# Kernel optimization log

Measured on AMD Instinct MI355X. Metric: run time of the kernel, lower is better.

## Reference

```python
import jax, jax.numpy as jnp
import numpy as np

H, DK, DV = 4, 64, 64        # heads, key/value head dims (hidden=256)
M, TOPK = 4, 2               # num memories, router top-k
GN, EPS, COND_SCALE = 16.0, 1e-5, 1.0


def setup_inputs() -> dict:
    key = jax.random.key(0)
    ks = jax.random.split(key, 12)
    B, Q, K, D = 8, 64, 256, 256
    w = lambda k, shape, fan: jax.random.normal(k, shape, jnp.float32) / np.sqrt(fan).astype(np.float32)
    return {
        "query": jax.random.normal(ks[0], (B, Q, D), jnp.float32),
        "keyval": jax.random.normal(ks[1], (B, K, D), jnp.float32),
        "attention_mask_kv": jnp.ones((B, K), jnp.int32),
        "W_cond": w(ks[2], (D, D), D),
        "W_q": w(ks[3], (D, H * DK), D),
        "W_k": w(ks[4], (D, H * DK), D),
        "W_v": w(ks[5], (D, H * DV), D),
        "W_gk1": w(ks[6], (D, 16), D),
        "W_gk2": w(ks[7], (16, H * DK), 16),
        "b_gk2": jnp.zeros((H * DK,), jnp.float32),
        "W_router": w(ks[8], (D, M), D),
        "norm_w": jnp.ones((DV,), jnp.float32),
        "W_o": w(ks[9], (H * DV, D), H * DV),
    }


def _mem_last(q_last, k, v, gk, sel, wgt):
    """Last-token output of one gated linear-attention memory.
    S_t = diag(exp(gk_t)) S_{t-1} + k_t v_t^T ; o_T = q_T S_T.
    q_last: (N,H,DK); k,gk: (N,K,H,DK); v: (N,K,H,DV); sel,wgt: (N,K)."""
    k_e = k * sel[:, :, None, None]
    v_e = v * wgt[:, :, None, None]
    gk_e = gk * sel[:, :, None, None]          # unselected tokens: no decay, no update
    G = jnp.cumsum(gk_e, axis=1)               # (N,K,H,DK), log decays
    decay = jnp.exp(G[:, -1:, :, :] - G)       # remaining decay to last step, <= 1
    s = jnp.einsum('nhd,nthd->nth', q_last, k_e * decay)
    return jnp.einsum('nth,nthv->nhv', s, v_e)


def reference(query, keyval, attention_mask_kv, W_cond, W_q, W_k, W_v,
              W_gk1, W_gk2, b_gk2, W_router, norm_w, W_o):
    B, Q, D = query.shape
    K = keyval.shape[1]
    N = B * Q
    # broadcast KV expansion + cond injection
    cond = (query @ W_cond) * COND_SCALE                         # (B,Q,D)
    x = (keyval[:, None, :, :] + cond[:, :, None, :]).reshape(N, K, D)
    m = jnp.broadcast_to(attention_mask_kv[:, None, :].astype(x.dtype), (B, Q, K)).reshape(N, K)
    # projections
    q = (x @ W_q).reshape(N, K, H, DK)
    k = (x @ W_k).reshape(N, K, H, DK) * m[:, :, None, None]
    v = (x @ W_v).reshape(N, K, H, DV) * m[:, :, None, None]
    gk = (jax.nn.log_sigmoid(x @ W_gk1 @ W_gk2 + b_gk2) / GN).reshape(N, K, H, DK)
    gk = gk * m[:, :, None, None]
    # router: softmax -> top-k -> renormalize
    router_logits = (x @ W_router).reshape(N * K, M)
    probs = jax.nn.softmax(router_logits, axis=-1)
    topv, topi = jax.lax.top_k(probs, TOPK)
    topv = topv / jnp.sum(topv, axis=-1, keepdims=True)
    w_mem = jnp.sum(jax.nn.one_hot(topi, M, dtype=x.dtype) * topv[..., None], axis=-2)
    w_mem = w_mem.reshape(N, K, M)
    # shared memory (always on) + routed memories
    q_last = q[:, -1]
    ones = jnp.ones((N, K), x.dtype)
    o = _mem_last(q_last, k, v, gk, ones, ones)
    for e in range(M):
        we = w_mem[:, :, e]
        o = o + _mem_last(q_last, k, v, gk, (we > 0).astype(x.dtype), we)
    # per-head RMSNorm + output projection
    o = o * jax.lax.rsqrt(jnp.mean(o * o, axis=-1, keepdims=True) + EPS) * norm_w
    out = (o.reshape(N, H * DV) @ W_o).reshape(B, Q, D)
    return out, router_logits
```

## Files before the change

### kernel.cpp

```cpp
#include <hip/hip_runtime.h>
#include <math.h>

#define Bb   8
#define Qq   64
#define Kk   256
#define Dd   256
#define Nn   (Bb * Qq)
#define GNi  0.0625f
#define EPSf 1e-5f

__device__ __forceinline__ float wred(float x) {
#pragma unroll
    for (int off = 32; off > 0; off >>= 1)
        x += __shfl_xor(x, off, 64);
    return x;
}

template<int R>
__device__ __forceinline__ void gemm64(
    const float* __restrict__ A, int lda,
    const float* __restrict__ B0, const float* __restrict__ B1,
    const float* __restrict__ B2, const float* __restrict__ B3,
    int bn, int Kc, float (&acc)[R][16], float* As, float* Ws)
{
    const int tid = threadIdx.x;
    const int aRow = tid >> 2, aCol = (tid & 3) * 4;
    const int wr = tid >> 4, wcb = (tid & 15) * 4;
    const int ty = tid >> 4, tx = tid & 15;
    const float* Bp[4] = {B0, B1, B2, B3};

    float4 rA = *(const float4*)(A + (size_t)aRow * lda + aCol);
    float4 rW[R];
#pragma unroll
    for (int r = 0; r < R; ++r)
        rW[r] = *(const float4*)(Bp[r] + (size_t)wr * 256 + bn + wcb);

    for (int k0 = 0; k0 < Kc; k0 += 16) {
        __syncthreads();
        As[(aCol + 0) * 68 + aRow] = rA.x;
        As[(aCol + 1) * 68 + aRow] = rA.y;
        As[(aCol + 2) * 68 + aRow] = rA.z;
        As[(aCol + 3) * 68 + aRow] = rA.w;
#pragma unroll
        for (int r = 0; r < R; ++r)
            *(float4*)&Ws[r * 1088 + wr * 68 + wcb] = rW[r];
        __syncthreads();
        if (k0 + 16 < Kc) {
            rA = *(const float4*)(A + (size_t)aRow * lda + k0 + 16 + aCol);
#pragma unroll
            for (int r = 0; r < R; ++r)
                rW[r] = *(const float4*)(Bp[r] + (size_t)(k0 + 16 + wr) * 256 + bn + wcb);
        }
#pragma unroll
        for (int kk = 0; kk < 16; ++kk) {
            const float4 a4 = *(const float4*)&As[kk * 68 + ty * 4];
            const float av[4] = {a4.x, a4.y, a4.z, a4.w};
#pragma unroll
            for (int r = 0; r < R; ++r) {
                const float4 b4 = *(const float4*)&Ws[r * 1088 + kk * 68 + tx * 4];
                const float bw[4] = {b4.x, b4.y, b4.z, b4.w};
#pragma unroll
                for (int i = 0; i < 4; ++i)
#pragma unroll
                    for (int j = 0; j < 4; ++j)
                        acc[r][i * 4 + j] = fmaf(av[i], bw[j], acc[r][i * 4 + j]);
            }
        }
    }
}

__global__ __launch_bounds__(256) void prep(
    const float* __restrict__ query, const float* __restrict__ keyval,
    const float* __restrict__ W_cond, const float* __restrict__ Wg1,
    const float* __restrict__ Wg2, const float* __restrict__ Wr,
    const float* __restrict__ Wq,
    float* __restrict__ cond, float* __restrict__ Wg,
    float* __restrict__ KVr, float* __restrict__ KVq8)
{
    __shared__ float lds[2 * 1088];
    const int id = blockIdx.x;
    const int tid = threadIdx.x;

    if (id < 48) {
        float acc[1][16] = {};
        const int ty = tid >> 4, tx = tid & 15;
        if (id < 32) {
            const int bm = (id >> 2) * 64, bn = (id & 3) * 64;
            gemm64<1>(query + (size_t)bm * Dd, Dd, W_cond, nullptr, nullptr, nullptr,
                      bn, Dd, acc, lds, lds + 1088);
#pragma unroll
            for (int i = 0; i < 4; ++i)
                *(float4*)&cond[(size_t)(bm + ty * 4 + i) * Dd + bn + tx * 4] =
                    make_float4(acc[0][i * 4 + 0], acc[0][i * 4 + 1],
                                acc[0][i * 4 + 2], acc[0][i * 4 + 3]);
        } else {
            const int id3 = id - 32;
            const int bm = (id3 >> 2) * 64, bn = (id3 & 3) * 64;
            gemm64<1>(Wg1 + (size_t)bm * 16, 16, Wg2, nullptr, nullptr, nullptr,
                      bn, 16, acc, lds, lds + 1088);
#pragma unroll
            for (int i = 0; i < 4; ++i)
                *(float4*)&Wg[(size_t)(bm + ty * 4 + i) * Dd + bn + tx * 4] =
                    make_float4(acc[0][i * 4 + 0], acc[0][i * 4 + 1],
                                acc[0][i * 4 + 2], acc[0][i * 4 + 3]);
        }
        return;
    }
    if (id < 80) {
        const int idx = (id - 48) * 256 + tid;
        const int row = idx >> 2, col = idx & 3;
        float a = 0.f;
        for (int k = 0; k < 256; ++k)
            a = fmaf(keyval[(size_t)row * Dd + k], Wr[(size_t)k * 4 + col], a);
        KVr[idx] = a;
        return;
    }
    for (int b8 = 0; b8 < 8; ++b8)
        lds[b8 * 256 + tid] = keyval[((size_t)b8 * Kk + 255) * Dd + tid];
    __syncthreads();
    float a8[8] = {};
    for (int k = 0; k < 256; ++k) {
        const float wq = Wq[(size_t)k * Dd + tid];
#pragma unroll
        for (int b8 = 0; b8 < 8; ++b8)
            a8[b8] = fmaf(lds[b8 * 256 + k], wq, a8[b8]);
    }
    for (int b8 = 0; b8 < 8; ++b8)
        KVq8[b8 * 256 + tid] = a8[b8];
}

__global__ __launch_bounds__(256) void maingemm(
    const float* __restrict__ keyval, const float* __restrict__ cond,
    const float* __restrict__ Wq, const float* __restrict__ Wk,
    const float* __restrict__ Wv, const float* __restrict__ Wg,
    const float* __restrict__ Wr,
    float* __restrict__ KVi, float* __restrict__ Cbi, float* __restrict__ Cr)
{
    __shared__ float lds[5 * 1088];
    const int id = blockIdx.x;
    const int tid = threadIdx.x;
    const int ty = tid >> 4, tx = tid & 15;

    if (id < 128) {
        const int bm = (id >> 2) * 64;
        const int bn = (id & 3) * 64;
        float acc[3][16] = {};
        gemm64<3>(keyval + (size_t)bm * Dd, Dd, Wk, Wv, Wg, nullptr,
                  bn, Dd, acc, lds, lds + 1088);
#pragma unroll
        for (int i = 0; i < 4; ++i) {
            const size_t rowo = (size_t)(bm + ty * 4 + i) * 1024;
#pragma unroll
            for (int j = 0; j < 4; ++j)
                *(float4*)&KVi[rowo + (size_t)(bn + tx * 4 + j) * 4] =
                    make_float4(acc[0][i * 4 + j], acc[1][i * 4 + j],
                                acc[2][i * 4 + j], 0.f);
        }
    } else if (id < 160) {
        const int id2 = id - 128;
        const int bm = (id2 >> 2) * 64;
        const int bn = (id2 & 3) * 64;
        float acc[4][16] = {};
        gemm64<4>(cond + (size_t)bm * Dd, Dd, Wq, Wk, Wv, Wg,
                  bn, Dd, acc, lds, lds + 1088);
#pragma unroll
        for (int i = 0; i < 4; ++i) {
            const size_t rowo = (size_t)(bm + ty * 4 + i) * 1024;
#pragma unroll
            for (int j = 0; j < 4; ++j)
                *(float4*)&Cbi[rowo + (size_t)(bn + tx * 4 + j) * 4] =
                    make_float4(acc[0][i * 4 + j], acc[1][i * 4 + j],
                                acc[2][i * 4 + j], acc[3][i * 4 + j]);
        }
    } else {
        const int idx = (id - 160) * 256 + tid;
        const int row = idx >> 2, col = idx & 3;
        float a = 0.f;
        for (int k = 0; k < 256; ++k)
            a = fmaf(cond[(size_t)row * Dd + k], Wr[(size_t)k * 4 + col], a);
        Cr[idx] = a;
    }
}

__device__ __forceinline__ void tile_step8(
    const float4* buf, int thi, const float* mfs, const float4* wm,
    float ql, float kc, float vc, float pc,
    float& E0, float& E1, float& E2, float& E3, float& E4, float& o,
    float (*Pt)[68], float* sb, int lane, int tl, int qq)
{
    float vreg[8];
#pragma unroll
    for (int i = 0; i < 8; ++i) {
        const int t = thi - i;
        const float mf = mfs[t];
        const float4 kv = buf[i];
        const float kkv = (kv.x + kc) * mf;
        vreg[i] = (kv.y + vc) * mf;
        const float pre = kv.z + pc;
        const float4 w = wm[t];
        const float ls = fminf(pre, 0.f) - __logf(1.f + __expf(-fabsf(pre)));
        float dg = __expf(ls * GNi);
        dg = (mf != 0.f) ? dg : 1.f;
        const float zf = (E0 + w.x * E1) + (w.y * E2 + w.z * E3) + w.w * E4;
        Pt[i][lane] = ql * kkv * zf;
        E0 *= dg;
        E1 *= (w.x > 0.f) ? dg : 1.f;
        E2 *= (w.y > 0.f) ? dg : 1.f;
        E3 *= (w.z > 0.f) ? dg : 1.f;
        E4 *= (w.w > 0.f) ? dg : 1.f;
    }
    __builtin_amdgcn_wave_barrier();
    const float4 p0 = *(const float4*)&Pt[tl][qq * 8];
    const float4 p1 = *(const float4*)&Pt[tl][qq * 8 + 4];
    float s = ((p0.x + p0.y) + (p0.z + p0.w)) + ((p1.x + p1.y) + (p1.z + p1.w));
    s += __shfl_xor(s, 8, 64);
    s += __shfl_xor(s, 16, 64);
    s += __shfl_xor(s, 32, 64);
    sb[tl] = s;
    __builtin_amdgcn_wave_barrier();
    const float4 s0 = *(const float4*)&sb[0];
    const float4 s1 = *(const float4*)&sb[4];
    o = fmaf(s0.x, vreg[0], o); o = fmaf(s0.y, vreg[1], o);
    o = fmaf(s0.z, vreg[2], o); o = fmaf(s0.w, vreg[3], o);
    o = fmaf(s1.x, vreg[4], o); o = fmaf(s1.y, vreg[5], o);
    o = fmaf(s1.z, vreg[6], o); o = fmaf(s1.w, vreg[7], o);
}

__global__ __launch_bounds__(256, 2) void mom_fused(
    const float4* __restrict__ KVi, const float* __restrict__ KVr,
    const float4* __restrict__ Cbi, const float* __restrict__ Cr,
    const float* __restrict__ KVq8, const float* __restrict__ b_gk2,
    const int* __restrict__ mask, const float* __restrict__ W_o,
    const float* __restrict__ norm_w,
    float* __restrict__ out, float* __restrict__ logits)
{
    __shared__ __align__(16) float4 wm[Kk];
    __shared__ __align__(16) float  mfs[Kk];
    __shared__ __align__(16) float  Ptile[4][8][68];
    __shared__ __align__(16) float  sbuf[4][8];
    __shared__ __align__(16) float  onorm[Dd];

    const int bi = blockIdx.x;
    const int n = (bi & 7) * 64 + (bi >> 3);
    const int b = bi & 7;
    const int j = threadIdx.x;
    const int lane = j & 63;
    const int wv = j >> 6;

    const float4 c4 = Cbi[(size_t)n * 256 + j];
    const float qc = c4.x, kc = c4.y, vc = c4.z;
    const float pc = c4.w + b_gk2[j];
    const float ql = KVq8[b * 256 + j] + qc;

    {
        mfs[j] = (float)mask[b * Kk + j];
        const float4 kvr = *(const float4*)&KVr[(size_t)(b * Kk + j) * 4];
        const float4 cr  = *(const float4*)&Cr[(size_t)n * 4];
        float l[4] = {kvr.x + cr.x, kvr.y + cr.y, kvr.z + cr.z, kvr.w + cr.w};
        *(float4*)(logits + ((size_t)n * Kk + j) * 4) =
            make_float4(l[0], l[1], l[2], l[3]);

        int i1 = 0;
#pragma unroll
        for (int q = 1; q < 4; ++q) if (l[q] > l[i1]) i1 = q;
        int i2 = -1;
#pragma unroll
        for (int q = 0; q < 4; ++q) {
            if (q == i1) continue;
            if (i2 < 0 || l[q] > l[i2]) i2 = q;
        }
        const float mx = fmaxf(l[i1], l[i2]);
        const float e1 = __expf(l[i1] - mx);
        const float e2 = __expf(l[i2] - mx);
        const float inv = 1.f / (e1 + e2);
        float w[4] = {0.f, 0.f, 0.f, 0.f};
        w[i1] = e1 * inv;
        w[i2] = e2 * inv;
        wm[j] = make_float4(w[0], w[1], w[2], w[3]);
    }
    __syncthreads();

    const float4* pkv = KVi + (size_t)b * Kk * 256 + j;

    float E0 = 1.f, E1 = 1.f, E2 = 1.f, E3 = 1.f, E4 = 1.f;
    float o = 0.f;
    const int tl = lane & 7, qq = lane >> 3;

    float4 bufA[8], bufB[8];
#pragma unroll
    for (int i = 0; i < 8; ++i) bufA[i] = pkv[(size_t)(255 - i) * 256];

    for (int p = 0; p < 16; ++p) {
        const int tA = 255 - 16 * p;
        const int tB = tA - 8;
#pragma unroll
        for (int i = 0; i < 8; ++i) bufB[i] = pkv[(size_t)(tB - i) * 256];
        tile_step8(bufA, tA, mfs, wm, ql, kc, vc, pc,
                   E0, E1, E2, E3, E4, o, Ptile[wv], sbuf[wv], lane, tl, qq);
        if (p < 15) {
#pragma unroll
            for (int i = 0; i < 8; ++i) bufA[i] = pkv[(size_t)(tB - 8 - i) * 256];
        }
        tile_step8(bufB, tB, mfs, wm, ql, kc, vc, pc,
                   E0, E1, E2, E3, E4, o, Ptile[wv], sbuf[wv], lane, tl, qq);
    }

    const float ms = wred(o * o) * (1.0f / 64.0f);
    onorm[j] = o * rsqrtf(ms + EPSf) * norm_w[lane];
    __syncthreads();

    float acc = 0.f;
#pragma unroll 8
    for (int k = 0; k < Dd; ++k)
        acc = fmaf(onorm[k], W_o[(size_t)k * Dd + j], acc);
    out[(size_t)n * Dd + j] = acc;
}

extern "C" void kernel_launch(void* const* d_in, const int* in_sizes, int n_in,
                              void* d_out, int out_size, void* d_ws, size_t ws_size,
                              hipStream_t stream)
{
    const float* query    = (const float*)d_in[0];
    const float* keyval   = (const float*)d_in[1];
    const int*   mask     = (const int*)  d_in[2];
    const float* W_cond   = (const float*)d_in[3];
    const float* W_q      = (const float*)d_in[4];
    const float* W_k      = (const float*)d_in[5];
    const float* W_v      = (const float*)d_in[6];
    const float* W_gk1    = (const float*)d_in[7];
    const float* W_gk2    = (const float*)d_in[8];
    const float* b_gk2    = (const float*)d_in[9];
    const float* W_router = (const float*)d_in[10];
    const float* norm_w   = (const float*)d_in[11];
    const float* W_o      = (const float*)d_in[12];

    float* out    = (float*)d_out;
    float* logits = out + Nn * Dd;

    float* p = (float*)d_ws;
    float* Wg   = p; p += Dd * Dd;
    float* cond = p; p += Nn * Dd;
    float* KVi  = p; p += (size_t)Bb * Kk * 1024;
    float* KVr  = p; p += Bb * Kk * 4;
    float* Cbi  = p; p += (size_t)Nn * 1024;
    float* Cr   = p; p += Nn * 4;
    float* KVq8 = p; p += Bb * Dd;

    prep<<<81, dim3(256), 0, stream>>>(
        query, keyval, W_cond, W_gk1, W_gk2, W_router, W_q,
        cond, Wg, KVr, KVq8);

    maingemm<<<168, dim3(256), 0, stream>>>(
        keyval, cond, W_q, W_k, W_v, Wg, W_router, KVi, Cbi, Cr);

    mom_fused<<<Nn, dim3(256), 0, stream>>>(
        (const float4*)KVi, KVr, (const float4*)Cbi, Cr,
        KVq8, b_gk2, mask, W_o, norm_w, out, logits);
}
```

Measured before the change: 212.2 us.

## Fuse three kernels into one persistent megakernel with grid barriers and prefolded weights

Replaces the prep, maingemm and mom_fused launches with a single 256-block, 512-thread kernel. Each block runs two independent 256-thread halves, and the three phases are separated by atomic-counter grid barriers. The cond activation is no longer materialized. W_cond is folded into W_q, W_k, W_v, the gate weights and the router weights, so the second phase multiplies the query directly by these combined weights. This removes launch gaps and the intermediate cond round trip, but relies on all 256 blocks being co-resident for the spin barrier and reduces per-block occupancy in the recurrence phase.

```diff
diff --git a/kernel.cpp b/kernel.cpp
--- a/kernel.cpp
+++ b/kernel.cpp
@@ -16,17 +16,26 @@
     return x;
 }
 
+__device__ __forceinline__ void grid_sync(unsigned* cnt, unsigned target) {
+    __syncthreads();
+    if (threadIdx.x == 0) {
+        __hip_atomic_fetch_add(cnt, 1u, __ATOMIC_ACQ_REL, __HIP_MEMORY_SCOPE_AGENT);
+        while (__hip_atomic_load(cnt, __ATOMIC_ACQUIRE, __HIP_MEMORY_SCOPE_AGENT) < target)
+            __builtin_amdgcn_s_sleep(8);
+    }
+    __syncthreads();
+}
+
 template<int R>
 __device__ __forceinline__ void gemm64(
-    const float* __restrict__ A, int lda,
+    int htid, const float* __restrict__ A, int lda,
     const float* __restrict__ B0, const float* __restrict__ B1,
     const float* __restrict__ B2, const float* __restrict__ B3,
     int bn, int Kc, float (&acc)[R][16], float* As, float* Ws)
 {
-    const int tid = threadIdx.x;
-    const int aRow = tid >> 2, aCol = (tid & 3) * 4;
-    const int wr = tid >> 4, wcb = (tid & 15) * 4;
-    const int ty = tid >> 4, tx = tid & 15;
+    const int aRow = htid >> 2, aCol = (htid & 3) * 4;
+    const int wr = htid >> 4, wcb = (htid & 15) * 4;
+    const int ty = htid >> 4, tx = htid & 15;
     const float* Bp[4] = {B0, B1, B2, B3};
 
     float4 rA = *(const float4*)(A + (size_t)aRow * lda + aCol);
@@ -66,119 +75,6 @@
                         acc[r][i * 4 + j] = fmaf(av[i], bw[j], acc[r][i * 4 + j]);
             }
         }
-    }
-}
-
-__global__ __launch_bounds__(256) void prep(
-    const float* __restrict__ query, const float* __restrict__ keyval,
-    const float* __restrict__ W_cond, const float* __restrict__ Wg1,
-    const float* __restrict__ Wg2, const float* __restrict__ Wr,
-    const float* __restrict__ Wq,
-    float* __restrict__ cond, float* __restrict__ Wg,
-    float* __restrict__ KVr, float* __restrict__ KVq8)
-{
-    __shared__ float lds[2 * 1088];
-    const int id = blockIdx.x;
-    const int tid = threadIdx.x;
-
-    if (id < 48) {
-        float acc[1][16] = {};
-        const int ty = tid >> 4, tx = tid & 15;
-        if (id < 32) {
-            const int bm = (id >> 2) * 64, bn = (id & 3) * 64;
-            gemm64<1>(query + (size_t)bm * Dd, Dd, W_cond, nullptr, nullptr, nullptr,
-                      bn, Dd, acc, lds, lds + 1088);
-#pragma unroll
-            for (int i = 0; i < 4; ++i)
-                *(float4*)&cond[(size_t)(bm + ty * 4 + i) * Dd + bn + tx * 4] =
-                    make_float4(acc[0][i * 4 + 0], acc[0][i * 4 + 1],
-                                acc[0][i * 4 + 2], acc[0][i * 4 + 3]);
-        } else {
-            const int id3 = id - 32;
-            const int bm = (id3 >> 2) * 64, bn = (id3 & 3) * 64;
-            gemm64<1>(Wg1 + (size_t)bm * 16, 16, Wg2, nullptr, nullptr, nullptr,
-                      bn, 16, acc, lds, lds + 1088);
-#pragma unroll
-            for (int i = 0; i < 4; ++i)
-                *(float4*)&Wg[(size_t)(bm + ty * 4 + i) * Dd + bn + tx * 4] =
-                    make_float4(acc[0][i * 4 + 0], acc[0][i * 4 + 1],
-                                acc[0][i * 4 + 2], acc[0][i * 4 + 3]);
-        }
-        return;
-    }
-    if (id < 80) {
-        const int idx = (id - 48) * 256 + tid;
-        const int row = idx >> 2, col = idx & 3;
-        float a = 0.f;
-        for (int k = 0; k < 256; ++k)
-            a = fmaf(keyval[(size_t)row * Dd + k], Wr[(size_t)k * 4 + col], a);
-        KVr[idx] = a;
-        return;
-    }
-    for (int b8 = 0; b8 < 8; ++b8)
-        lds[b8 * 256 + tid] = keyval[((size_t)b8 * Kk + 255) * Dd + tid];
-    __syncthreads();
-    float a8[8] = {};
-    for (int k = 0; k < 256; ++k) {
-        const float wq = Wq[(size_t)k * Dd + tid];
-#pragma unroll
-        for (int b8 = 0; b8 < 8; ++b8)
-            a8[b8] = fmaf(lds[b8 * 256 + k], wq, a8[b8]);
-    }
-    for (int b8 = 0; b8 < 8; ++b8)
-        KVq8[b8 * 256 + tid] = a8[b8];
-}
-
-__global__ __launch_bounds__(256) void maingemm(
-    const float* __restrict__ keyval, const float* __restrict__ cond,
-    const float* __restrict__ Wq, const float* __restrict__ Wk,
-    const float* __restrict__ Wv, const float* __restrict__ Wg,
-    const float* __restrict__ Wr,
-    float* __restrict__ KVi, float* __restrict__ Cbi, float* __restrict__ Cr)
-{
-    __shared__ float lds[5 * 1088];
-    const int id = blockIdx.x;
-    const int tid = threadIdx.x;
-    const int ty = tid >> 4, tx = tid & 15;
-
-    if (id < 128) {
-        const int bm = (id >> 2) * 64;
-        const int bn = (id & 3) * 64;
-        float acc[3][16] = {};
-        gemm64<3>(keyval + (size_t)bm * Dd, Dd, Wk, Wv, Wg, nullptr,
-                  bn, Dd, acc, lds, lds + 1088);
-#pragma unroll
-        for (int i = 0; i < 4; ++i) {
-            const size_t rowo = (size_t)(bm + ty * 4 + i) * 1024;
-#pragma unroll
-            for (int j = 0; j < 4; ++j)
-                *(float4*)&KVi[rowo + (size_t)(bn + tx * 4 + j) * 4] =
-                    make_float4(acc[0][i * 4 + j], acc[1][i * 4 + j],
-                                acc[2][i * 4 + j], 0.f);
-        }
-    } else if (id < 160) {
-        const int id2 = id - 128;
-        const int bm = (id2 >> 2) * 64;
-        const int bn = (id2 & 3) * 64;
-        float acc[4][16] = {};
-        gemm64<4>(cond + (size_t)bm * Dd, Dd, Wq, Wk, Wv, Wg,
-                  bn, Dd, acc, lds, lds + 1088);
-#pragma unroll
-        for (int i = 0; i < 4; ++i) {
-            const size_t rowo = (size_t)(bm + ty * 4 + i) * 1024;
-#pragma unroll
-            for (int j = 0; j < 4; ++j)
-                *(float4*)&Cbi[rowo + (size_t)(bn + tx * 4 + j) * 4] =
-                    make_float4(acc[0][i * 4 + j], acc[1][i * 4 + j],
-                                acc[2][i * 4 + j], acc[3][i * 4 + j]);
-        }
-    } else {
-        const int idx = (id - 160) * 256 + tid;
-        const int row = idx >> 2, col = idx & 3;
-        float a = 0.f;
-        for (int k = 0; k < 256; ++k)
-            a = fmaf(cond[(size_t)row * Dd + k], Wr[(size_t)k * 4 + col], a);
-        Cr[idx] = a;
     }
 }
 
@@ -226,28 +122,183 @@
     o = fmaf(s1.z, vreg[6], o); o = fmaf(s1.w, vreg[7], o);
 }
 
-__global__ __launch_bounds__(256, 2) void mom_fused(
-    const float4* __restrict__ KVi, const float* __restrict__ KVr,
-    const float4* __restrict__ Cbi, const float* __restrict__ Cr,
-    const float* __restrict__ KVq8, const float* __restrict__ b_gk2,
-    const int* __restrict__ mask, const float* __restrict__ W_o,
-    const float* __restrict__ norm_w,
+__global__ __launch_bounds__(512) void mega(
+    const float* __restrict__ query, const float* __restrict__ keyval,
+    const int* __restrict__ mask, const float* __restrict__ W_cond,
+    const float* __restrict__ Wq, const float* __restrict__ Wk,
+    const float* __restrict__ Wv, const float* __restrict__ Wg1,
+    const float* __restrict__ Wg2, const float* __restrict__ b_gk2,
+    const float* __restrict__ Wr, const float* __restrict__ norm_w,
+    const float* __restrict__ W_o,
+    float* __restrict__ Wg, float* __restrict__ Wpq, float* __restrict__ Wpk,
+    float* __restrict__ Wpv, float* __restrict__ Wpg, float* __restrict__ Wpr,
+    float* __restrict__ KVq8, float* __restrict__ KVr, float* __restrict__ KVi,
+    float* __restrict__ Cbi, float* __restrict__ Cr,
+    unsigned* __restrict__ cnt,
     float* __restrict__ out, float* __restrict__ logits)
 {
-    __shared__ __align__(16) float4 wm[Kk];
+    __shared__ __align__(16) float gA[2][1088];
+    __shared__ __align__(16) float gW[2][4 * 1088];
+    __shared__ __align__(16) float Tst[2][64 * 16];
+    __shared__ __align__(16) float4 wm[2][Kk];
     __shared__ __align__(16) float  mfs[Kk];
-    __shared__ __align__(16) float  Ptile[4][8][68];
-    __shared__ __align__(16) float  sbuf[4][8];
-    __shared__ __align__(16) float  onorm[Dd];
+    __shared__ __align__(16) float  Ptile[8][8][68];
+    __shared__ __align__(16) float  sbuf[8][8];
+    __shared__ __align__(16) float  onorm[2][Dd];
 
     const int bi = blockIdx.x;
-    const int n = (bi & 7) * 64 + (bi >> 3);
-    const int b = bi & 7;
-    const int j = threadIdx.x;
-    const int lane = j & 63;
-    const int wv = j >> 6;
-
-    const float4 c4 = Cbi[(size_t)n * 256 + j];
+    const int tid = threadIdx.x;
+    const int s = tid >> 8;
+    const int htid = tid & 255;
+    const int ty = htid >> 4, tx = htid & 15;
+
+    if (bi < 24) {
+        const int t = 2 * bi + s;
+        const float* Wm = (t < 16) ? Wq : (t < 32) ? Wk : Wv;
+        float* Wpm      = (t < 16) ? Wpq : (t < 32) ? Wpk : Wpv;
+        const int sub = t & 15;
+        const int bm = (sub >> 2) * 64, bn = (sub & 3) * 64;
+        float acc[1][16] = {};
+        gemm64<1>(htid, W_cond + (size_t)bm * 256, 256, Wm, nullptr, nullptr,
+                  nullptr, bn, 256, acc, gA[s], gW[s]);
+#pragma unroll
+        for (int i = 0; i < 4; ++i)
+            *(float4*)&Wpm[(size_t)(bm + ty * 4 + i) * 256 + bn + tx * 4] =
+                make_float4(acc[0][i * 4 + 0], acc[0][i * 4 + 1],
+                            acc[0][i * 4 + 2], acc[0][i * 4 + 3]);
+    } else if (bi < 32) {
+        const int t = 2 * (bi - 24) + s;
+        const int bm = (t >> 2) * 64, bn = (t & 3) * 64;
+        float acc[1][16] = {};
+        gemm64<1>(htid, Wg1 + (size_t)bm * 16, 16, Wg2, nullptr, nullptr,
+                  nullptr, bn, 16, acc, gA[s], gW[s]);
+#pragma unroll
+        for (int i = 0; i < 4; ++i)
+            *(float4*)&Wg[(size_t)(bm + ty * 4 + i) * 256 + bn + tx * 4] =
+                make_float4(acc[0][i * 4 + 0], acc[0][i * 4 + 1],
+                            acc[0][i * 4 + 2], acc[0][i * 4 + 3]);
+    } else if (bi < 40) {
+        const int t = 2 * (bi - 32) + s;
+        const int bm = (t >> 2) * 64, bn = (t & 3) * 64;
+        {
+            const int r = htid >> 2, g = htid & 3;
+            float4 a4 = make_float4(0.f, 0.f, 0.f, 0.f);
+            for (int k = 0; k < 256; ++k) {
+                const float a = W_cond[(size_t)(bm + r) * 256 + k];
+                const float4 w4 = *(const float4*)&Wg1[(size_t)k * 16 + g * 4];
+                a4.x = fmaf(a, w4.x, a4.x);
+                a4.y = fmaf(a, w4.y, a4.y);
+                a4.z = fmaf(a, w4.z, a4.z);
+                a4.w = fmaf(a, w4.w, a4.w);
+            }
+            *(float4*)&Tst[s][r * 16 + g * 4] = a4;
+        }
+        __syncthreads();
+        {
+            float o16[16] = {};
+#pragma unroll
+            for (int i16 = 0; i16 < 16; ++i16) {
+                const float4 w4 = *(const float4*)&Wg2[(size_t)i16 * 256 + bn + tx * 4];
+#pragma unroll
+                for (int i = 0; i < 4; ++i) {
+                    const float tv = Tst[s][(ty * 4 + i) * 16 + i16];
+                    o16[i * 4 + 0] = fmaf(tv, w4.x, o16[i * 4 + 0]);
+                    o16[i * 4 + 1] = fmaf(tv, w4.y, o16[i * 4 + 1]);
+                    o16[i * 4 + 2] = fmaf(tv, w4.z, o16[i * 4 + 2]);
+                    o16[i * 4 + 3] = fmaf(tv, w4.w, o16[i * 4 + 3]);
+                }
+            }
+#pragma unroll
+            for (int i = 0; i < 4; ++i)
+                *(float4*)&Wpg[(size_t)(bm + ty * 4 + i) * 256 + bn + tx * 4] =
+                    make_float4(o16[i * 4 + 0], o16[i * 4 + 1],
+                                o16[i * 4 + 2], o16[i * 4 + 3]);
+        }
+    } else if (bi == 40) {
+        if (s == 0) {
+            float4 a4 = make_float4(0.f, 0.f, 0.f, 0.f);
+            for (int k = 0; k < 256; ++k) {
+                const float a = W_cond[(size_t)htid * 256 + k];
+                const float4 w4 = *(const float4*)&Wr[(size_t)k * 4];
+                a4.x = fmaf(a, w4.x, a4.x);
+                a4.y = fmaf(a, w4.y, a4.y);
+                a4.z = fmaf(a, w4.z, a4.z);
+                a4.w = fmaf(a, w4.w, a4.w);
+            }
+            *(float4*)&Wpr[(size_t)htid * 4] = a4;
+        } else {
+            float a8[8] = {};
+            for (int k = 0; k < 256; ++k) {
+                const float wqv = Wq[(size_t)k * 256 + htid];
+#pragma unroll
+                for (int b8 = 0; b8 < 8; ++b8)
+                    a8[b8] = fmaf(keyval[((size_t)b8 * Kk + 255) * 256 + k], wqv, a8[b8]);
+            }
+#pragma unroll
+            for (int b8 = 0; b8 < 8; ++b8)
+                KVq8[b8 * 256 + htid] = a8[b8];
+        }
+    } else if (bi < 57) {
+        const int idx = (bi - 41) * 512 + tid;
+        const int row = idx >> 2, col = idx & 3;
+        float a = 0.f;
+        for (int k = 0; k < 256; ++k)
+            a = fmaf(keyval[(size_t)row * 256 + k], Wr[(size_t)k * 4 + col], a);
+        KVr[idx] = a;
+    }
+
+    grid_sync(cnt, 256);
+
+    if (bi < 80) {
+        const int t = 2 * bi + s;
+        if (t < 128) {
+            const int bm = (t >> 2) * 64, bn = (t & 3) * 64;
+            float acc[3][16] = {};
+            gemm64<3>(htid, keyval + (size_t)bm * 256, 256, Wk, Wv, Wg,
+                      nullptr, bn, 256, acc, gA[s], gW[s]);
+#pragma unroll
+            for (int i = 0; i < 4; ++i) {
+                const size_t rowo = (size_t)(bm + ty * 4 + i) * 1024;
+#pragma unroll
+                for (int j = 0; j < 4; ++j)
+                    *(float4*)&KVi[rowo + (size_t)(bn + tx * 4 + j) * 4] =
+                        make_float4(acc[0][i * 4 + j], acc[1][i * 4 + j],
+                                    acc[2][i * 4 + j], 0.f);
+            }
+        } else {
+            const int t2 = t - 128;
+            const int bm = (t2 >> 2) * 64, bn = (t2 & 3) * 64;
+            float acc[4][16] = {};
+            gemm64<4>(htid, query + (size_t)bm * 256, 256, Wpq, Wpk, Wpv, Wpg,
+                      bn, 256, acc, gA[s], gW[s]);
+#pragma unroll
+            for (int i = 0; i < 4; ++i) {
+                const size_t rowo = (size_t)(bm + ty * 4 + i) * 1024;
+#pragma unroll
+                for (int j = 0; j < 4; ++j)
+                    *(float4*)&Cbi[rowo + (size_t)(bn + tx * 4 + j) * 4] =
+                        make_float4(acc[0][i * 4 + j], acc[1][i * 4 + j],
+                                    acc[2][i * 4 + j], acc[3][i * 4 + j]);
+            }
+        }
+    } else if (bi < 84) {
+        const int idx = (bi - 80) * 512 + tid;
+        const int row = idx >> 2, col = idx & 3;
+        float a = 0.f;
+        for (int k = 0; k < 256; ++k)
+            a = fmaf(query[(size_t)row * 256 + k], Wpr[(size_t)k * 4 + col], a);
+        Cr[idx] = a;
+    }
+
+    grid_sync(cnt, 512);
+
+    const int n = 2 * bi + s;
+    const int b = bi >> 5;
+    const int j = htid;
+    const int lane = tid & 63;
+    const int wv = tid >> 6;
+
+    const float4 c4 = *(const float4*)&Cbi[(size_t)n * 1024 + j * 4];
     const float qc = c4.x, kc = c4.y, vc = c4.z;
     const float pc = c4.w + b_gk2[j];
     const float ql = KVq8[b * 256 + j] + qc;
@@ -276,11 +327,11 @@
         float w[4] = {0.f, 0.f, 0.f, 0.f};
         w[i1] = e1 * inv;
         w[i2] = e2 * inv;
-        wm[j] = make_float4(w[0], w[1], w[2], w[3]);
+        wm[s][j] = make_float4(w[0], w[1], w[2], w[3]);
     }
     __syncthreads();
 
-    const float4* pkv = KVi + (size_t)b * Kk * 256 + j;
+    const float4* pkv = (const float4*)KVi + (size_t)b * Kk * 256 + j;
 
     float E0 = 1.f, E1 = 1.f, E2 = 1.f, E3 = 1.f, E4 = 1.f;
     float o = 0.f;
@@ -295,24 +346,24 @@
         const int tB = tA - 8;
 #pragma unroll
         for (int i = 0; i < 8; ++i) bufB[i] = pkv[(size_t)(tB - i) * 256];
-        tile_step8(bufA, tA, mfs, wm, ql, kc, vc, pc,
+        tile_step8(bufA, tA, mfs, wm[s], ql, kc, vc, pc,
                    E0, E1, E2, E3, E4, o, Ptile[wv], sbuf[wv], lane, tl, qq);
         if (p < 15) {
 #pragma unroll
             for (int i = 0; i < 8; ++i) bufA[i] = pkv[(size_t)(tB - 8 - i) * 256];
         }
-        tile_step8(bufB, tB, mfs, wm, ql, kc, vc, pc,
+        tile_step8(bufB, tB, mfs, wm[s], ql, kc, vc, pc,
                    E0, E1, E2, E3, E4, o, Ptile[wv], sbuf[wv], lane, tl, qq);
     }
 
     const float ms = wred(o * o) * (1.0f / 64.0f);
-    onorm[j] = o * rsqrtf(ms + EPSf) * norm_w[lane];
+    onorm[s][j] = o * rsqrtf(ms + EPSf) * norm_w[j & 63];
     __syncthreads();
 
     float acc = 0.f;
 #pragma unroll 8
     for (int k = 0; k < Dd; ++k)
-        acc = fmaf(onorm[k], W_o[(size_t)k * Dd + j], acc);
+        acc = fmaf(onorm[s][k], W_o[(size_t)k * Dd + j], acc);
     out[(size_t)n * Dd + j] = acc;
 }
 
@@ -337,23 +388,25 @@
     float* out    = (float*)d_out;
     float* logits = out + Nn * Dd;
 
-    float* p = (float*)d_ws;
+    unsigned* cnt = (unsigned*)d_ws;
+    float* p = (float*)((char*)d_ws + 64);
     float* Wg   = p; p += Dd * Dd;
-    float* cond = p; p += Nn * Dd;
+    float* Wpq  = p; p += Dd * Dd;
+    float* Wpk  = p; p += Dd * Dd;
+    float* Wpv  = p; p += Dd * Dd;
+    float* Wpg  = p; p += Dd * Dd;
+    float* Wpr  = p; p += Dd * 4;
+    float* KVq8 = p; p += Bb * Dd;
+    float* KVr  = p; p += Bb * Kk * 4;
     float* KVi  = p; p += (size_t)Bb * Kk * 1024;
-    float* KVr  = p; p += Bb * Kk * 4;
     float* Cbi  = p; p += (size_t)Nn * 1024;
     float* Cr   = p; p += Nn * 4;
-    float* KVq8 = p; p += Bb * Dd;
-
-    prep<<<81, dim3(256), 0, stream>>>(
-        query, keyval, W_cond, W_gk1, W_gk2, W_router, W_q,
-        cond, Wg, KVr, KVq8);
-
-    maingemm<<<168, dim3(256), 0, stream>>>(
-        keyval, cond, W_q, W_k, W_v, Wg, W_router, KVi, Cbi, Cr);
-
-    mom_fused<<<Nn, dim3(256), 0, stream>>>(
-        (const float4*)KVi, KVr, (const float4*)Cbi, Cr,
-        KVq8, b_gk2, mask, W_o, norm_w, out, logits);
-}
+
+    hipMemsetAsync(d_ws, 0, 64, stream);
+
+    mega<<<256, dim3(512), 0, stream>>>(
+        query, keyval, mask, W_cond, W_q, W_k, W_v, W_gk1, W_gk2, b_gk2,
+        W_router, norm_w, W_o,
+        Wg, Wpq, Wpk, Wpv, Wpg, Wpr, KVq8, KVr, KVi, Cbi, Cr,
+        cnt, out, logits);
+}
```

After: 848.4 us. 300% more time.
